# Performance work log

Measured on AMD Instinct MI355X. Metric: run time of the kernel, lower is better.

Reference implementation:

```python
import jax, jax.numpy as jnp
import numpy as np

B, N, ENC = 64, 49, 2048   # batch, num feature pixels, encoder dim
S = 26                     # caption length (S-1 decode steps)
V, E, H, A = 10000, 512, 512, 512  # vocab, embed, hidden, attention dims


def setup_inputs() -> dict:
    key = jax.random.key(0)
    ks = jax.random.split(key, 20)
    g = lambda k, shape, fan_in: jax.random.normal(k, shape, jnp.float32) / np.sqrt(fan_in)
    return {
        "features": jax.random.normal(ks[0], (B, N, ENC), jnp.float32),
        "captions": jax.random.randint(ks[1], (B, S), 0, V),
        "emb": g(ks[2], (V, E), E),
        # LSTMCell: gate order i, f, g, o (PyTorch convention)
        "W_ih": g(ks[3], (4 * H, E + ENC), E + ENC),
        "b_ih": jnp.zeros((4 * H,), jnp.float32),
        "W_hh": g(ks[4], (4 * H, H), H),
        "b_hh": jnp.zeros((4 * H,), jnp.float32),
        "W_enc_att": g(ks[5], (A, ENC), ENC),
        "b_enc_att": jnp.zeros((A,), jnp.float32),
        "W_dec_att": g(ks[6], (A, H), H),
        "b_dec_att": jnp.zeros((A,), jnp.float32),
        "W_full": g(ks[7], (1, A), A),
        "b_full": jnp.zeros((1,), jnp.float32),
        "W_init_h": g(ks[8], (H, ENC), ENC),
        "b_init_h": jnp.zeros((H,), jnp.float32),
        "W_init_c": g(ks[9], (H, ENC), ENC),
        "b_init_c": jnp.zeros((H,), jnp.float32),
        "W_fcn": g(ks[10], (V, H), H),
        "b_fcn": jnp.zeros((V,), jnp.float32),
    }


def _forward(features, captions, emb, W_ih, b_ih, W_hh, b_hh,
             W_enc_att, b_enc_att, W_dec_att, b_dec_att, W_full, b_full,
             W_init_h, b_init_h, W_init_c, b_init_c, W_fcn, b_fcn):
    embeds = emb[captions]                         # [B, S, E]
    mean_enc = features.mean(axis=1)               # [B, ENC]
    h = mean_enc @ W_init_h.T + b_init_h           # [B, H]
    c = mean_enc @ W_init_c.T + b_init_c
    att1 = features @ W_enc_att.T + b_enc_att      # [B, N, A] (loop-invariant)

    def step(carry, x_s):
        h, c = carry
        att2 = h @ W_dec_att.T + b_dec_att                      # [B, A]
        e = jax.nn.relu(att1 + att2[:, None, :]) @ W_full.T + b_full  # [B, N, 1]
        alpha = jax.nn.softmax(e, axis=1)                       # [B, N, 1]
        context = (features * alpha).sum(axis=1)                # [B, ENC]
        x = jnp.concatenate([x_s, context], axis=1)             # [B, E+ENC]
        gates = x @ W_ih.T + b_ih + h @ W_hh.T + b_hh           # [B, 4H]
        i, f, g_, o = jnp.split(gates, 4, axis=1)
        c_new = jax.nn.sigmoid(f) * c + jax.nn.sigmoid(i) * jnp.tanh(g_)
        h_new = jax.nn.sigmoid(o) * jnp.tanh(c_new)
        pred = h_new @ W_fcn.T + b_fcn                          # [B, V] (dropout = identity, eval mode)
        return (h_new, c_new), (pred, alpha[..., 0])

    xs = jnp.swapaxes(embeds[:, : S - 1], 0, 1)    # [S-1, B, E]
    (_, _), (preds, alphas) = jax.lax.scan(step, (h, c), xs)
    preds = jnp.swapaxes(preds, 0, 1)              # [B, S-1, V]
    alphas = jnp.swapaxes(alphas, 0, 1)            # [B, S-1, N]
    return preds, alphas


def reference(features, captions, emb, W_ih, b_ih, W_hh, b_hh,
              W_enc_att, b_enc_att, W_dec_att, b_dec_att, W_full, b_full,
              W_init_h, b_init_h, W_init_c, b_init_c, W_fcn, b_fcn):
    return _forward(features, captions, emb, W_ih, b_ih, W_hh, b_hh,
                    W_enc_att, b_enc_att, W_dec_att, b_dec_att, W_full, b_full,
                    W_init_h, b_init_h, W_init_c, b_init_c, W_fcn, b_fcn)
```

## Files before the change

kernel.cpp:

```cpp
#include <hip/hip_runtime.h>
#include <hip/hip_bf16.h>
#include <math.h>

typedef __bf16 bf16;
typedef __bf16 bf16x4 __attribute__((ext_vector_type(4)));
typedef __bf16 bf16x8 __attribute__((ext_vector_type(8)));
typedef float f32x4 __attribute__((ext_vector_type(4)));
typedef _Float16 f16;
typedef _Float16 f16x4 __attribute__((ext_vector_type(4)));
typedef _Float16 f16x8 __attribute__((ext_vector_type(8)));

#define BB 64
#define NN 49
#define CENC 2048
#define SS 26
#define NSTEP 25
#define VV 10000
#define EE 512
#define HH 512
#define AAT 512
#define ALPHA_OFF (BB*NSTEP*VV)
#define NPROD 40
#define NCONS 128


struct Wks {
  unsigned int flagP; unsigned int _p0[31];
  unsigned int flagH; unsigned int _p1[31];
  f16  att1_16[BB*NN*AAT];
  float c0[BB*HH];
  f16  h16t[BB*HH];
  float hw[BB*2560];
  float embg[NSTEP*BB*4*HH];
  union {
    f16 fg16[BB*NN*4*HH];
    struct {
      bf16 Wfcn_hi[10048*HH];
      bf16 Winh_hi[HH*CENC];
      bf16 Winc_hi[HH*CENC];
    } w;
  } u;
  f16  Wcomb16[2560*HH];
  bf16 mean_hi[BB*CENC];
  bf16 mean_lo[BB*CENC];
  bf16 xemb_hi[NSTEP*BB*EE];
  bf16 xemb_lo[NSTEP*BB*EE];
  bf16 hist_hi[NSTEP*BB*HH];
  bf16 hist_lo[NSTEP*BB*HH];
  bf16 Wih_hi[4*HH*(EE+CENC)];
  bf16 Wih_lo[4*HH*(EE+CENC)];
  bf16 Wenc_hi[AAT*CENC];
};

__device__ inline bf16x8 ldb8(const bf16* p){ return *(const bf16x8*)p; }
__device__ inline f32x4 mfma16(bf16x8 a, bf16x8 b, f32x4 c){
  return __builtin_amdgcn_mfma_f32_16x16x32_bf16(a, b, c, 0, 0, 0);
}
__device__ inline f32x4 mfma16f(f16x8 a, f16x8 b, f32x4 c){
  return __builtin_amdgcn_mfma_f32_16x16x32_f16(a, b, c, 0, 0, 0);
}
__device__ inline float sigm(float x){ return 1.0f/(1.0f+expf(-x)); }

__device__ inline void wait_ge(unsigned int* f, unsigned int target){
  while (__hip_atomic_load(f, __ATOMIC_RELAXED, __HIP_MEMORY_SCOPE_AGENT) < target)
    __builtin_amdgcn_s_sleep(2);
  (void)__hip_atomic_load(f, __ATOMIC_ACQUIRE, __HIP_MEMORY_SCOPE_AGENT);
}

__device__ inline void split8(const float* p, bf16x8& hi, bf16x8& lo){
  float4 v0 = *(const float4*)p;
  float4 v1 = *(const float4*)(p+4);
  float v[8] = {v0.x,v0.y,v0.z,v0.w,v1.x,v1.y,v1.z,v1.w};
  #pragma unroll
  for (int j=0;j<8;j++){ bf16 h=(bf16)v[j]; hi[j]=h; lo[j]=(bf16)(v[j]-(float)h); }
}

__device__ inline void gll16(const bf16* g, bf16* l){
  __builtin_amdgcn_global_load_lds(
      (const __attribute__((address_space(1))) void*)g,
      (__attribute__((address_space(3))) void*)l, 16, 0, 0);
}

__global__ __launch_bounds__(256) void k_cvt_sw(const float* __restrict__ src,
    bf16* __restrict__ hi, bf16* __restrict__ lo, int R, int K, int ntile){
  int g = blockIdx.x*256 + threadIdx.x;
  if (g >= ntile*64) return;
  int tile = g>>6, lane = g&63;
  int KC = K>>5;
  int rt = tile/KC, kc = tile - rt*KC;
  int r = rt*16 + (lane&15);
  if (r >= R) r = R-1;
  int k = kc*32 + (lane>>4)*8;
  bf16x8 hv, lv;
  split8(src + (size_t)r*K + k, hv, lv);
  *(bf16x8*)(hi + (size_t)g*8) = hv;
  if (lo) *(bf16x8*)(lo + (size_t)g*8) = lv;
}

__global__ __launch_bounds__(256) void k_cvt_sw16(const float* __restrict__ src,
    f16* __restrict__ dst, int R, int K, int ntile){
  int g = blockIdx.x*256 + threadIdx.x;
  if (g >= ntile*64) return;
  int tile = g>>6, lane = g&63;
  int KC = K>>5;
  int rt = tile/KC, kc = tile - rt*KC;
  int r = rt*16 + (lane&15);
  if (r >= R) r = R-1;
  int k = kc*32 + (lane>>4)*8;
  float4 v0 = *(const float4*)(src + (size_t)r*K + k);
  float4 v1 = *(const float4*)(src + (size_t)r*K + k + 4);
  float v[8] = {v0.x,v0.y,v0.z,v0.w,v1.x,v1.y,v1.z,v1.w};
  f16x8 hv;
  #pragma unroll
  for (int j=0;j<8;j++) hv[j] = (f16)v[j];
  *(f16x8*)(dst + (size_t)g*8) = hv;
}

__global__ __launch_bounds__(256) void k_emb(const int* __restrict__ caps,
    const float* __restrict__ emb, Wks* __restrict__ ws){
  int g = blockIdx.x*256 + threadIdx.x;
  if (g >= 1600*64) return;
  int tile = g>>6, lane = g&63;
  int rt = tile>>4, kc = tile&15;
  int r = rt*16 + (lane&15);
  int s = r>>6, b = r&63;
  int k = kc*32 + (lane>>4)*8;
  int cap = caps[b*SS + s];
  bf16x8 hv, lv;
  split8(emb + (size_t)cap*EE + k, hv, lv);
  *(bf16x8*)(ws->xemb_hi + (size_t)g*8) = hv;
  *(bf16x8*)(ws->xemb_lo + (size_t)g*8) = lv;
}

__global__ __launch_bounds__(256) void k_mean(const float* __restrict__ feat, Wks* __restrict__ ws){
  int idx = blockIdx.x*256 + threadIdx.x;
  int b = idx >> 11, ch = idx & 2047;
  const float* p = feat + (size_t)b*NN*CENC + ch;
  float s = 0.f;
  #pragma unroll
  for (int n=0;n<NN;n++) s += p[n*CENC];
  s *= (1.0f/49.0f);
  bf16 hi = (bf16)s;
  int off = (((b>>4)*64 + (ch>>5))*64 + ((ch&31)>>3)*16 + (b&15))*8 + (ch&7);
  ws->mean_hi[off] = hi;
  ws->mean_lo[off] = (bf16)(s - (float)hi);
}

__global__ __launch_bounds__(256) void k_init(Wks* __restrict__ ws,
    const float* __restrict__ bh, const float* __restrict__ bc){
  if (blockIdx.x == 0 && threadIdx.x == 0){ ws->flagP = 0u; ws->flagH = 0u; }
  int wid = threadIdx.x >> 6, lane = threadIdx.x & 63;
  int w = blockIdx.x*4 + wid;
  int mat = w >> 5, nt = w & 31;
  int lane15 = lane & 15, quad = lane >> 4;
  const bf16* Wm = mat ? ws->u.w.Winc_hi : ws->u.w.Winh_hi;
  const float* bm = mat ? bc : bh;
  int col = nt*16 + lane15;
  f32x4 acc[4] = {};
  for (int kc=0; kc<64; kc++){
    bf16x8 bfr = ldb8(Wm + (((size_t)nt*64 + kc)*64 + lane)*8);
    #pragma unroll
    for (int t=0;t<4;t++){
      acc[t] = mfma16(ldb8(ws->mean_hi + (((size_t)t*64 + kc)*64 + lane)*8), bfr, acc[t]);
      acc[t] = mfma16(ldb8(ws->mean_lo + (((size_t)t*64 + kc)*64 + lane)*8), bfr, acc[t]);
    }
  }
  float bias = bm[col];
  #pragma unroll
  for (int t=0;t<4;t++){
    #pragma unroll
    for (int r=0;r<4;r++){
      int b = t*16 + quad*4 + r;
      float v = acc[t][r] + bias;
      if (mat == 0){
        int kc2 = col>>5, lane_w = ((col&31)>>3)*16 + (b&15), j8 = col&7;
        ws->h16t[(((b>>4)*16 + kc2)*64 + lane_w)*8 + j8] = (f16)v;
      } else {
        ws->c0[b*HH + col] = v;
      }
    }
  }
}

__global__ __launch_bounds__(256) void k_embg(Wks* __restrict__ ws,
    const float* __restrict__ bih, const float* __restrict__ bhh){
  int wid = threadIdx.x>>6, lane = threadIdx.x&63;
  int w = blockIdx.x*4 + wid;
  int nt = w/25, mtg = w - nt*25;
  int lane15 = lane&15, quad = lane>>4;
  f32x4 acc[4] = {};
  for (int kc=0; kc<16; kc++){
    bf16x8 wh = ldb8(ws->Wih_hi + (((size_t)nt*80 + kc)*64 + lane)*8);
    bf16x8 wl = ldb8(ws->Wih_lo + (((size_t)nt*80 + kc)*64 + lane)*8);
    #pragma unroll
    for (int i=0;i<4;i++){
      int rt = mtg*4 + i;
      bf16x8 ah = ldb8(ws->xemb_hi + (((size_t)rt*16 + kc)*64 + lane)*8);
      bf16x8 al = ldb8(ws->xemb_lo + (((size_t)rt*16 + kc)*64 + lane)*8);
      acc[i] = mfma16(ah, wh, acc[i]);
      acc[i] = mfma16(al, wh, acc[i]);
      acc[i] = mfma16(ah, wl, acc[i]);
    }
  }
  int col = nt*16 + lane15;
  float bias = bih[col] + bhh[col];
  #pragma unroll
  for (int i=0;i<4;i++){
    #pragma unroll
    for (int r=0;r<4;r++){
      int row = (mtg*4+i)*16 + quad*4 + r;
      ws->embg[(size_t)row*(4*HH) + col] = acc[i][r] + bias;
    }
  }
}

__global__ __launch_bounds__(256) void k_enc(const float* __restrict__ feat,
    const float* __restrict__ benc, Wks* __restrict__ ws)
{
  __shared__ bf16 sm[2][24*512];
  int xcd = blockIdx.x & 7, idx = blockIdx.x >> 3;
  int wg = (xcd < 4) ? xcd*123 + idx : 4*123 + (xcd-4)*122 + idx;
  int mb = wg / 20, nb = wg % 20;
  int tid = threadIdx.x, wid = tid>>6, lane = tid&63;
  int lane15 = lane&15, quad = lane>>4;
  bool is_fg = (nb < 16);
  int rr = tid>>2, qo = tid&3;
  const float* arow = feat + (size_t)(mb*64 + rr)*CENC + qo*8;
  int a_ds = ((rr>>4)*2)*512 + (qo*16 + (rr&15))*8;

  f32x4 acc[8] = {};

  auto stageB = [&](int kc, int buf){
    if (is_fg){
      #pragma unroll
      for (int j=0;j<4;j++){
        int tt = wid*4 + j;
        int ntl = tt>>1;
        const bf16* src = ((tt&1) ? ws->Wih_lo : ws->Wih_hi)
            + (size_t)((nb*8 + ntl)*80 + 16 + kc)*512 + lane*8;
        gll16(src, &sm[buf][(8+tt)*512]);
      }
    } else {
      #pragma unroll
      for (int j=0;j<2;j++){
        int tt = wid*2 + j;
        const bf16* src = ws->Wenc_hi
            + (size_t)(((nb-16)*8 + tt)*64 + kc)*512 + lane*8;
        gll16(src, &sm[buf][(8+tt)*512]);
      }
    }
  };
  auto cvtwr = [&](int buf, float4 v0, float4 v1){
    float v[8] = {v0.x,v0.y,v0.z,v0.w,v1.x,v1.y,v1.z,v1.w};
    bf16x8 hv, lv;
    #pragma unroll
    for (int j=0;j<8;j++){ bf16 h=(bf16)v[j]; hv[j]=h; lv[j]=(bf16)(v[j]-(float)h); }
    *(bf16x8*)(&sm[buf][a_ds]) = hv;
    *(bf16x8*)(&sm[buf][a_ds+512]) = lv;
  };

  stageB(0, 0);
  { float4 v0 = *(const float4*)arow;
    float4 v1 = *(const float4*)(arow+4);
    cvtwr(0, v0, v1); }
  __syncthreads();

  for (int kc=0; kc<64; kc++){
    int cur = kc & 1;
    bool pf = (kc < 63);
    float4 v0, v1;
    if (pf){
      stageB(kc+1, cur^1);
      const float* p = arow + (kc+1)*32;
      v0 = *(const float4*)p; v1 = *(const float4*)(p+4);
    }
    const bf16* S = sm[cur];
    bf16x8 ah = ldb8(S + (wid*2)*512 + lane*8);
    bf16x8 al = ldb8(S + (wid*2+1)*512 + lane*8);
    if (is_fg){
      #pragma unroll
      for (int u=0;u<8;u++){
        bf16x8 wh = ldb8(S + (size_t)(8+u*2)*512 + lane*8);
        bf16x8 wl = ldb8(S + (size_t)(9+u*2)*512 + lane*8);
        acc[u] = mfma16(ah, wh, acc[u]);
        acc[u] = mfma16(al, wh, acc[u]);
        acc[u] = mfma16(ah, wl, acc[u]);
      }
    } else {
      #pragma unroll
      for (int u=0;u<8;u++){
        bf16x8 wh = ldb8(S + (size_t)(8+u)*512 + lane*8);
        acc[u] = mfma16(ah, wh, acc[u]);
        acc[u] = mfma16(al, wh, acc[u]);
      }
    }
    if (pf) cvtwr(cur^1, v0, v1);
    __syncthreads();
  }

  if (is_fg){
    #pragma unroll
    for (int u=0;u<8;u++){
      int col = nb*128 + u*16 + lane15;
      #pragma unroll
      for (int r=0;r<4;r++){
        int row = mb*64 + wid*16 + quad*4 + r;
        ws->u.fg16[(size_t)row*(4*HH) + col] = (f16)acc[u][r];
      }
    }
  } else {
    #pragma unroll
    for (int u=0;u<8;u++){
      int col = (nb-16)*128 + u*16 + lane15;
      float bias = benc[col];
      #pragma unroll
      for (int r=0;r<4;r++){
        int row = mb*64 + wid*16 + quad*4 + r;
        ws->att1_16[(size_t)row*AAT + col] = (f16)(acc[u][r] + bias);
      }
    }
  }
}

__global__ __launch_bounds__(256) void k_steps(Wks* __restrict__ ws,
    const float* __restrict__ bdec, const float* __restrict__ Wfull,
    float* __restrict__ out)
{
  __shared__ __align__(16) unsigned char smem[161280];
  int blk = blockIdx.x;
  int tid = threadIdx.x;
  int lane = tid & 63, wid = tid >> 6;
  int lane15 = lane & 15, quad = lane >> 4;

  if (blk < NPROD){
    f16* h_s = (f16*)smem;
    f16* w_s = (f16*)(smem + 65536);
    const f16* wsrc = ws->Wcomb16 + (size_t)blk*32768;
    for (int i = tid; i < 4096; i += 256)
      *(f16x8*)(w_s + (size_t)i*8) = *(const f16x8*)(wsrc + (size_t)i*8);
    for (int t=0; t<NSTEP; t++){
      if (t>0 && tid==0) wait_ge(&ws->flagH, (unsigned)(NCONS*t));
      __syncthreads();
      for (int i = tid; i < 4096; i += 256)
        *(f16x8*)(h_s + (size_t)i*8) = *(const f16x8*)(ws->h16t + (size_t)i*8);
      __syncthreads();
      f32x4 acc[4] = {};
      for (int kc=0; kc<16; kc++){
        f16x8 wv = *(const f16x8*)(w_s + ((size_t)(wid*16 + kc)*64 + lane)*8);
        #pragma unroll
        for (int rt=0;rt<4;rt++){
          f16x8 hv = *(const f16x8*)(h_s + ((size_t)(rt*16 + kc)*64 + lane)*8);
          acc[rt] = mfma16f(hv, wv, acc[rt]);
        }
      }
      int col = blk*64 + wid*16 + lane15;
      #pragma unroll
      for (int rt=0;rt<4;rt++){
        #pragma unroll
        for (int r=0;r<4;r++)
          ws->hw[(size_t)(rt*16 + quad*4 + r)*2560 + col] = acc[rt][r];
      }
      __syncthreads();
      if (tid==0)
        __hip_atomic_fetch_add(&ws->flagP, 1u, __ATOMIC_RELEASE,
                               __HIP_MEMORY_SCOPE_AGENT);
    }
    return;
  }

  f16*   att1_s = (f16*)smem;
  f16*   fg_s   = (f16*)(smem + 50176);
  float* att2_s = (float*)(smem + 150528);
  float* wf_s   = (float*)(smem + 152576);
  float* bd_s   = (float*)(smem + 154624);
  float* g_s    = (float*)(smem + 156672);
  float* e_s    = (float*)(smem + 160768);
  float* al_s   = (float*)(smem + 161024);
  int cb = blk - NPROD;
  int b = cb >> 1, jh = cb & 1;
  for (int i = tid; i < NN*64; i += 256)
    *(f16x8*)(att1_s + (size_t)i*8) =
        *(const f16x8*)(ws->att1_16 + ((size_t)b*NN*64 + i)*8);
  for (int i = tid; i < NN*4*32; i += 256){
    int n = i >> 7, rem = i & 127, g2 = rem >> 5, c8 = rem & 31;
    *(f16x8*)(fg_s + (((n<<2) + g2)<<8) + c8*8) =
        *(const f16x8*)(ws->u.fg16 + (size_t)(b*NN+n)*2048 + g2*512 + jh*256 + c8*8);
  }
  wf_s[tid] = Wfull[tid]; wf_s[tid+256] = Wfull[tid+256];
  bd_s[tid] = bdec[tid];  bd_s[tid+256] = bdec[tid+256];
  float c_reg = ws->c0[b*HH + jh*256 + tid];
  int g = tid>>6, i4 = (tid&63)*4;
  int gc = g*512 + jh*256 + i4;
  int col = jh*256 + tid;
  int kc = col>>5, lane_w = ((col&31)>>3)*16 + (b&15), j8 = col&7;
  int offh = (((b>>4)*16 + kc)*64 + lane_w)*8 + j8;
  __syncthreads();

  for (int t=0; t<NSTEP; t++){
    float4 ev = *(const float4*)(ws->embg + (size_t)(t*64+b)*2048 + gc);
    if (tid==0) wait_ge(&ws->flagP, (unsigned)(NPROD*(t+1)));
    __syncthreads();
    att2_s[tid]     = ws->hw[(size_t)b*2560 + 2048 + tid]       + bd_s[tid];
    att2_s[tid+256] = ws->hw[(size_t)b*2560 + 2048 + 256 + tid] + bd_s[tid+256];
    float4 gacc;
    {
      float4 hv4 = *(const float4*)(ws->hw + (size_t)b*2560 + gc);
      gacc.x = ev.x + hv4.x;
      gacc.y = ev.y + hv4.y;
      gacc.z = ev.z + hv4.z;
      gacc.w = ev.w + hv4.w;
    }
    __syncthreads();
    for (int n = wid; n < NN; n += 4){
      f16x8 a1v = *(const f16x8*)(att1_s + n*512 + lane*8);
      float s = 0.f;
      #pragma unroll
      for (int j=0;j<8;j++){
        float v = (float)a1v[j] + att2_s[lane*8+j];
        v = fmaxf(v, 0.f);
        s += v * wf_s[lane*8+j];
      }
      #pragma unroll
      for (int off=32; off; off>>=1) s += __shfl_xor(s, off, 64);
      if (lane==0) e_s[n] = s;
    }
    __syncthreads();
    if (wid==0){
      float e = (lane < NN) ? e_s[lane] : -1e30f;
      float m = e;
      #pragma unroll
      for (int off=32; off; off>>=1) m = fmaxf(m, __shfl_xor(m, off, 64));
      float p = (lane < NN) ? expf(e - m) : 0.f;
      float su = p;
      #pragma unroll
      for (int off=32; off; off>>=1) su += __shfl_xor(su, off, 64);
      float al = p/su;
      if (lane < NN){
        al_s[lane] = al;
        if (jh==0) out[ALPHA_OFF + (size_t)(b*NSTEP + t)*NN + lane] = al;
      }
    }
    __syncthreads();
    {
      const f16* fp_ = fg_s + (g<<8) + i4;
      #pragma unroll 7
      for (int n=0;n<NN;n++){
        float a = al_s[n];
        f16x4 v = *(const f16x4*)(fp_ + (size_t)n*1024);
        gacc.x += a*(float)v[0];
        gacc.y += a*(float)v[1];
        gacc.z += a*(float)v[2];
        gacc.w += a*(float)v[3];
      }
      *(float4*)(g_s + (g<<8) + i4) = gacc;
    }
    __syncthreads();
    {
      float iv = g_s[tid], fv = g_s[256+tid], gv = g_s[512+tid], ov = g_s[768+tid];
      float cn = sigm(fv)*c_reg + sigm(iv)*tanhf(gv);
      float hn = sigm(ov)*tanhf(cn);
      c_reg = cn;
      ws->h16t[offh] = (f16)hn;
      bf16 hi_ = (bf16)hn;
      bf16 lo_ = (bf16)(hn - (float)hi_);
      size_t offhist = ((((size_t)t*4 + (b>>4))*16 + kc)*64 + lane_w)*8 + j8;
      ws->hist_hi[offhist] = hi_;
      ws->hist_lo[offhist] = lo_;
    }
    __syncthreads();
    if (tid==0)
      __hip_atomic_fetch_add(&ws->flagH, 1u, __ATOMIC_RELEASE,
                             __HIP_MEMORY_SCOPE_AGENT);
  }
}

__global__ __launch_bounds__(256) void k_pred(Wks* __restrict__ ws,
    const float* __restrict__ bfcn, float* __restrict__ out)
{
  int wid = threadIdx.x>>6, lane = threadIdx.x&63;
  int mt = blockIdx.y*4 + wid;
  int nt = blockIdx.x;
  if (mt >= NSTEP) return;
  int lane15 = lane&15, quad = lane>>4;
  int n0 = nt*64;
  f32x4 acc[4][4] = {};
  for (int kc=0; kc<16; kc++){
    bf16x8 a_hi[4], a_lo[4], bw[4];
    #pragma unroll
    for (int i=0;i<4;i++){
      a_hi[i] = ldb8(ws->hist_hi + (((size_t)(mt*4+i)*16 + kc)*64 + lane)*8);
      a_lo[i] = ldb8(ws->hist_lo + (((size_t)(mt*4+i)*16 + kc)*64 + lane)*8);
    }
    #pragma unroll
    for (int u=0;u<4;u++)
      bw[u] = ldb8(ws->u.w.Wfcn_hi + (((size_t)(nt*4+u)*16 + kc)*64 + lane)*8);
    #pragma unroll
    for (int u=0;u<4;u++){
      #pragma unroll
      for (int i=0;i<4;i++){
        acc[u][i] = mfma16(a_hi[i], bw[u], acc[u][i]);
        acc[u][i] = mfma16(a_lo[i], bw[u], acc[u][i]);
      }
    }
  }
  #pragma unroll
  for (int u=0;u<4;u++){
    int vc = n0 + u*16 + lane15;
    if (vc < VV){
      float bias = bfcn[vc];
      #pragma unroll
      for (int i=0;i<4;i++){
        #pragma unroll
        for (int r=0;r<4;r++){
          int row = mt*64 + i*16 + quad*4 + r;
          int sstep = row >> 6, bidx = row & 63;
          out[(size_t)(bidx*NSTEP + sstep)*VV + vc] = acc[u][i][r] + bias;
        }
      }
    }
  }
}

extern "C" void kernel_launch(void* const* d_in, const int* in_sizes, int n_in,
                              void* d_out, int out_size, void* d_ws, size_t ws_size,
                              hipStream_t stream)
{
  const float* feat = (const float*)d_in[0];
  const int*   caps = (const int*)d_in[1];
  const float* emb  = (const float*)d_in[2];
  const float* Wih  = (const float*)d_in[3];
  const float* bih  = (const float*)d_in[4];
  const float* Whh  = (const float*)d_in[5];
  const float* bhh  = (const float*)d_in[6];
  const float* Wenc = (const float*)d_in[7];
  const float* benc = (const float*)d_in[8];
  const float* Wdec = (const float*)d_in[9];
  const float* bdec = (const float*)d_in[10];
  const float* Wfull= (const float*)d_in[11];
  const float* bfull= (const float*)d_in[12];
  const float* Winh = (const float*)d_in[13];
  const float* binh = (const float*)d_in[14];
  const float* Winc = (const float*)d_in[15];
  const float* binc = (const float*)d_in[16];
  const float* Wfcn = (const float*)d_in[17];
  const float* bfcn = (const float*)d_in[18];
  float* out = (float*)d_out;
  Wks* ws = (Wks*)d_ws;
  if (ws_size < sizeof(Wks)) return;
  (void)bfull;

  #define SW(src, hi, lo, R, K) do { int nt_ = ((R+15)/16)*((K)/32); \
    hipLaunchKernelGGL(k_cvt_sw, dim3((nt_*64+255)/256), dim3(256), 0, stream, \
        src, hi, lo, R, K, nt_); } while(0)
  SW(Wih,  ws->Wih_hi,  ws->Wih_lo,  2048, 2560);
  SW(Wenc, ws->Wenc_hi, (bf16*)nullptr, 512, 2048);
  SW(Winh, ws->u.w.Winh_hi, (bf16*)nullptr, 512, 2048);
  SW(Winc, ws->u.w.Winc_hi, (bf16*)nullptr, 512, 2048);
  hipLaunchKernelGGL(k_cvt_sw16, dim3((128*16*64+255)/256), dim3(256), 0, stream,
      Whh, ws->Wcomb16, 2048, 512, 128*16);
  hipLaunchKernelGGL(k_cvt_sw16, dim3((32*16*64+255)/256), dim3(256), 0, stream,
      Wdec, ws->Wcomb16 + (size_t)2048*512, 512, 512, 32*16);
  hipLaunchKernelGGL(k_emb, dim3(400), dim3(256), 0, stream, caps, emb, ws);
  hipLaunchKernelGGL(k_mean, dim3(512), dim3(256), 0, stream, feat, ws);
  hipLaunchKernelGGL(k_init, dim3(16), dim3(256), 0, stream, ws, binh, binc);
  hipLaunchKernelGGL(k_embg, dim3(800), dim3(256), 0, stream, ws, bih, bhh);
  hipLaunchKernelGGL(k_enc, dim3(980), dim3(256), 0, stream, feat, benc, ws);
  hipLaunchKernelGGL(k_steps, dim3(NPROD+NCONS), dim3(256), 0, stream,
      ws, bdec, Wfull, out);
  SW(Wfcn, ws->u.w.Wfcn_hi, (bf16*)nullptr, 10000, 512);
  #undef SW
  hipLaunchKernelGGL(k_pred, dim3(157, 7), dim3(256), 0, stream, ws, bfcn, out);
}
```

Before: 1.107 ms.

## Remove producer blocks; compute recurrent matvec per batch pair with pairwise flags

The separate producer blocks that computed h@[W_hh;W_dec] for all batches, and the global all-to-all flag barriers between producers and consumers, are removed. Each consumer block pair now computes its own batch row's recurrent gates and attention projection with MFMA, reading weights directly from global/L2. The two halves of a batch exchange their h halves through global memory with a pairwise flag. This replaces a grid-wide handshake per step with local pair sync, but each block now streams about 2.5 MB of f16 weights per step from L2 and uses only one valid MFMA row out of 16.

```diff
diff --git a/kernel.cpp b/kernel.cpp
--- a/kernel.cpp
+++ b/kernel.cpp
@@ -20,17 +20,14 @@
 #define HH 512
 #define AAT 512
 #define ALPHA_OFF (BB*NSTEP*VV)
-#define NPROD 40
 #define NCONS 128
 
 
 struct Wks {
-  unsigned int flagP; unsigned int _p0[31];
-  unsigned int flagH; unsigned int _p1[31];
+  unsigned int pairflag[BB][2][32];
   f16  att1_16[BB*NN*AAT];
   float c0[BB*HH];
-  f16  h16t[BB*HH];
-  float hw[BB*2560];
+  f16  h16x[BB*HH];
   float embg[NSTEP*BB*4*HH];
   union {
     f16 fg16[BB*NN*4*HH];
@@ -61,12 +58,6 @@
 }
 __device__ inline float sigm(float x){ return 1.0f/(1.0f+expf(-x)); }
 
-__device__ inline void wait_ge(unsigned int* f, unsigned int target){
-  while (__hip_atomic_load(f, __ATOMIC_RELAXED, __HIP_MEMORY_SCOPE_AGENT) < target)
-    __builtin_amdgcn_s_sleep(2);
-  (void)__hip_atomic_load(f, __ATOMIC_ACQUIRE, __HIP_MEMORY_SCOPE_AGENT);
-}
-
 __device__ inline void split8(const float* p, bf16x8& hi, bf16x8& lo){
   float4 v0 = *(const float4*)p;
   float4 v1 = *(const float4*)(p+4);
@@ -148,7 +139,8 @@
 
 __global__ __launch_bounds__(256) void k_init(Wks* __restrict__ ws,
     const float* __restrict__ bh, const float* __restrict__ bc){
-  if (blockIdx.x == 0 && threadIdx.x == 0){ ws->flagP = 0u; ws->flagH = 0u; }
+  if (blockIdx.x == 0 && threadIdx.x < 128)
+    ws->pairflag[threadIdx.x>>1][threadIdx.x&1][0] = 0u;
   int wid = threadIdx.x >> 6, lane = threadIdx.x & 63;
   int w = blockIdx.x*4 + wid;
   int mat = w >> 5, nt = w & 31;
@@ -172,12 +164,8 @@
     for (int r=0;r<4;r++){
       int b = t*16 + quad*4 + r;
       float v = acc[t][r] + bias;
-      if (mat == 0){
-        int kc2 = col>>5, lane_w = ((col&31)>>3)*16 + (b&15), j8 = col&7;
-        ws->h16t[(((b>>4)*16 + kc2)*64 + lane_w)*8 + j8] = (f16)v;
-      } else {
-        ws->c0[b*HH + col] = v;
-      }
+      if (mat == 0) ws->h16x[(size_t)b*HH + col] = (f16)v;
+      else          ws->c0[b*HH + col] = v;
     }
   }
 }
@@ -326,58 +314,19 @@
     const float* __restrict__ bdec, const float* __restrict__ Wfull,
     float* __restrict__ out)
 {
-  __shared__ __align__(16) unsigned char smem[161280];
-  int blk = blockIdx.x;
-  int tid = threadIdx.x;
-  int lane = tid & 63, wid = tid >> 6;
-  int lane15 = lane & 15, quad = lane >> 4;
-
-  if (blk < NPROD){
-    f16* h_s = (f16*)smem;
-    f16* w_s = (f16*)(smem + 65536);
-    const f16* wsrc = ws->Wcomb16 + (size_t)blk*32768;
-    for (int i = tid; i < 4096; i += 256)
-      *(f16x8*)(w_s + (size_t)i*8) = *(const f16x8*)(wsrc + (size_t)i*8);
-    for (int t=0; t<NSTEP; t++){
-      if (t>0 && tid==0) wait_ge(&ws->flagH, (unsigned)(NCONS*t));
-      __syncthreads();
-      for (int i = tid; i < 4096; i += 256)
-        *(f16x8*)(h_s + (size_t)i*8) = *(const f16x8*)(ws->h16t + (size_t)i*8);
-      __syncthreads();
-      f32x4 acc[4] = {};
-      for (int kc=0; kc<16; kc++){
-        f16x8 wv = *(const f16x8*)(w_s + ((size_t)(wid*16 + kc)*64 + lane)*8);
-        #pragma unroll
-        for (int rt=0;rt<4;rt++){
-          f16x8 hv = *(const f16x8*)(h_s + ((size_t)(rt*16 + kc)*64 + lane)*8);
-          acc[rt] = mfma16f(hv, wv, acc[rt]);
-        }
-      }
-      int col = blk*64 + wid*16 + lane15;
-      #pragma unroll
-      for (int rt=0;rt<4;rt++){
-        #pragma unroll
-        for (int r=0;r<4;r++)
-          ws->hw[(size_t)(rt*16 + quad*4 + r)*2560 + col] = acc[rt][r];
-      }
-      __syncthreads();
-      if (tid==0)
-        __hip_atomic_fetch_add(&ws->flagP, 1u, __ATOMIC_RELEASE,
-                               __HIP_MEMORY_SCOPE_AGENT);
-    }
-    return;
-  }
-
+  __shared__ __align__(16) unsigned char smem[162304];
   f16*   att1_s = (f16*)smem;
   f16*   fg_s   = (f16*)(smem + 50176);
-  float* att2_s = (float*)(smem + 150528);
-  float* wf_s   = (float*)(smem + 152576);
-  float* bd_s   = (float*)(smem + 154624);
-  float* g_s    = (float*)(smem + 156672);
-  float* e_s    = (float*)(smem + 160768);
-  float* al_s   = (float*)(smem + 161024);
-  int cb = blk - NPROD;
-  int b = cb >> 1, jh = cb & 1;
+  f16*   h_s    = (f16*)(smem + 150528);
+  float* hw_s   = (float*)(smem + 151552);
+  float* wf_s   = (float*)(smem + 157696);
+  float* bd_s   = (float*)(smem + 159744);
+  float* e_s    = (float*)(smem + 161792);
+  float* al_s   = (float*)(smem + 162048);
+  int blk = blockIdx.x, tid = threadIdx.x;
+  int lane = tid & 63, wid = tid >> 6, quad = lane >> 4;
+  int b = blk >> 1, jh = blk & 1;
+
   for (int i = tid; i < NN*64; i += 256)
     *(f16x8*)(att1_s + (size_t)i*8) =
         *(const f16x8*)(ws->att1_16 + ((size_t)b*NN*64 + i)*8);
@@ -388,35 +337,71 @@
   }
   wf_s[tid] = Wfull[tid]; wf_s[tid+256] = Wfull[tid+256];
   bd_s[tid] = bdec[tid];  bd_s[tid+256] = bdec[tid+256];
+  if (tid < 64)
+    *(f16x8*)(h_s + tid*8) = *(const f16x8*)(ws->h16x + (size_t)b*HH + tid*8);
   float c_reg = ws->c0[b*HH + jh*256 + tid];
   int g = tid>>6, i4 = (tid&63)*4;
   int gc = g*512 + jh*256 + i4;
   int col = jh*256 + tid;
-  int kc = col>>5, lane_w = ((col&31)>>3)*16 + (b&15), j8 = col&7;
-  int offh = (((b>>4)*16 + kc)*64 + lane_w)*8 + j8;
+  int kcc = col>>5, lane_w = ((col&31)>>3)*16 + (b&15), j8 = col&7;
   __syncthreads();
 
   for (int t=0; t<NSTEP; t++){
     float4 ev = *(const float4*)(ws->embg + (size_t)(t*64+b)*2048 + gc);
-    if (tid==0) wait_ge(&ws->flagP, (unsigned)(NPROD*(t+1)));
+    f16x8 af[16];
+    #pragma unroll
+    for (int k2=0;k2<16;k2++)
+      af[k2] = *(const f16x8*)(h_s + k2*32 + quad*8);
+    for (int g4=0; g4<6; g4++){
+      int wt[4], dst[4];
+      #pragma unroll
+      for (int u=0;u<4;u++){
+        int tt = wid*24 + g4*4 + u;
+        if (tt < 64){ int gg=tt>>4, uu=tt&15; wt[u]=gg*32+jh*16+uu; dst[u]=gg*256+uu*16; }
+        else        { wt[u]=128+(tt-64); dst[u]=1024+(tt-64)*16; }
+      }
+      f32x4 a0={}, a1={}, a2={}, a3={};
+      #pragma unroll
+      for (int k2=0;k2<16;k2++){
+        const f16* base = ws->Wcomb16 + (size_t)k2*512 + (size_t)lane*8;
+        f16x8 b0 = *(const f16x8*)(base + (size_t)wt[0]*8192);
+        f16x8 b1 = *(const f16x8*)(base + (size_t)wt[1]*8192);
+        f16x8 b2 = *(const f16x8*)(base + (size_t)wt[2]*8192);
+        f16x8 b3 = *(const f16x8*)(base + (size_t)wt[3]*8192);
+        a0 = mfma16f(af[k2], b0, a0);
+        a1 = mfma16f(af[k2], b1, a1);
+        a2 = mfma16f(af[k2], b2, a2);
+        a3 = mfma16f(af[k2], b3, a3);
+      }
+      if (lane < 16){
+        float v0 = a0[0], v1 = a1[0], v2 = a2[0], v3 = a3[0];
+        if (dst[0] >= 1024){
+          v0 += bd_s[dst[0]-1024+lane];
+          v1 += bd_s[dst[1]-1024+lane];
+          v2 += bd_s[dst[2]-1024+lane];
+          v3 += bd_s[dst[3]-1024+lane];
+        }
+        hw_s[dst[0]+lane] = v0;
+        hw_s[dst[1]+lane] = v1;
+        hw_s[dst[2]+lane] = v2;
+        hw_s[dst[3]+lane] = v3;
+      }
+    }
     __syncthreads();
-    att2_s[tid]     = ws->hw[(size_t)b*2560 + 2048 + tid]       + bd_s[tid];
-    att2_s[tid+256] = ws->hw[(size_t)b*2560 + 2048 + 256 + tid] + bd_s[tid+256];
     float4 gacc;
     {
-      float4 hv4 = *(const float4*)(ws->hw + (size_t)b*2560 + gc);
+      float4 hv4 = *(const float4*)(hw_s + g*256 + i4);
       gacc.x = ev.x + hv4.x;
       gacc.y = ev.y + hv4.y;
       gacc.z = ev.z + hv4.z;
       gacc.w = ev.w + hv4.w;
     }
-    __syncthreads();
     for (int n = wid; n < NN; n += 4){
       f16x8 a1v = *(const f16x8*)(att1_s + n*512 + lane*8);
       float s = 0.f;
       #pragma unroll
       for (int j=0;j<8;j++){
-        float v = (float)a1v[j] + att2_s[lane*8+j];
+        float v = (float)a1v[j] + hw_s[1024 + lane*8 + j];
         v = fmaxf(v, 0.f);
         s += v * wf_s[lane*8+j];
       }
@@ -452,25 +437,55 @@
         gacc.z += a*(float)v[2];
         gacc.w += a*(float)v[3];
       }
-      *(float4*)(g_s + (g<<8) + i4) = gacc;
+      *(float4*)(hw_s + (g<<8) + i4) = gacc;
     }
     __syncthreads();
     {
-      float iv = g_s[tid], fv = g_s[256+tid], gv = g_s[512+tid], ov = g_s[768+tid];
+      float iv = hw_s[tid], fv = hw_s[256+tid], gv = hw_s[512+tid], ov = hw_s[768+tid];
       float cn = sigm(fv)*c_reg + sigm(iv)*tanhf(gv);
       float hn = sigm(ov)*tanhf(cn);
       c_reg = cn;
-      ws->h16t[offh] = (f16)hn;
+      h_s[col] = (f16)hn;
       bf16 hi_ = (bf16)hn;
       bf16 lo_ = (bf16)(hn - (float)hi_);
-      size_t offhist = ((((size_t)t*4 + (b>>4))*16 + kc)*64 + lane_w)*8 + j8;
+      size_t offhist = ((((size_t)t*4 + (b>>4))*16 + kcc)*64 + lane_w)*8 + j8;
       ws->hist_hi[offhist] = hi_;
       ws->hist_lo[offhist] = lo_;
     }
     __syncthreads();
-    if (tid==0)
-      __hip_atomic_fetch_add(&ws->flagH, 1u, __ATOMIC_RELEASE,
-                             __HIP_MEMORY_SCOPE_AGENT);
+    if (t < NSTEP-1){
+      if (tid < 32){
+        f32x4 hv = *(const f32x4*)((const char*)h_s + jh*512 + tid*16);
+        asm volatile("global_store_dwordx4 %0, %1, off sc0 sc1"
+            :: "v"((char*)ws->h16x + (size_t)b*1024 + jh*512 + tid*16), "v"(hv)
+            : "memory");
+        asm volatile("s_waitcnt vmcnt(0)" ::: "memory");
+      }
+      __syncthreads();
+      if (tid == 0){
+        unsigned fl = (unsigned)(t+1);
+        asm volatile("global_store_dword %0, %1, off sc0 sc1"
+            :: "v"(&ws->pairflag[b][jh][0]), "v"(fl) : "memory");
+        unsigned got = 0;
+        do {
+          __builtin_amdgcn_s_sleep(1);
+          asm volatile("global_load_dword %0, %1, off sc0 sc1"
+              : "=v"(got) : "v"(&ws->pairflag[b][jh^1][0]));
+          asm volatile("s_waitcnt vmcnt(0)" ::: "memory");
+        } while (got <= (unsigned)t);
+      }
+      __syncthreads();
+      if (tid < 32){
+        f32x4 hv;
+        asm volatile("global_load_dwordx4 %0, %1, off sc0 sc1"
+            : "=v"(hv)
+            : "v"((const char*)ws->h16x + (size_t)b*1024 + (jh^1)*512 + tid*16));
+        asm volatile("s_waitcnt vmcnt(0)" ::: "memory");
+        __builtin_amdgcn_sched_barrier(0);
+        *(f32x4*)((char*)h_s + (jh^1)*512 + tid*16) = hv;
+      }
+      __syncthreads();
+    }
   }
 }
 
@@ -565,7 +580,7 @@
   hipLaunchKernelGGL(k_init, dim3(16), dim3(256), 0, stream, ws, binh, binc);
   hipLaunchKernelGGL(k_embg, dim3(800), dim3(256), 0, stream, ws, bih, bhh);
   hipLaunchKernelGGL(k_enc, dim3(980), dim3(256), 0, stream, feat, benc, ws);
-  hipLaunchKernelGGL(k_steps, dim3(NPROD+NCONS), dim3(256), 0, stream,
+  hipLaunchKernelGGL(k_steps, dim3(NCONS), dim3(256), 0, stream,
       ws, bdec, Wfull, out);
   SW(Wfcn, ws->u.w.Wfcn_hi, (bf16*)nullptr, 10000, 512);
   #undef SW
```

After: 1.153 ms. 1.04x slower.
